# Optimization experiments

Hardware: AMD Instinct MI355X
Metric: run time of the kernel (lower is better)

The kernel has to match this reference:

```python
import jax, jax.numpy as jnp
import numpy as np

NUM_HEADS = 8


def setup_inputs() -> dict:
    key = jax.random.key(0)
    ks = jax.random.split(key, 5)
    b, c, h, w = 8, 256, 32, 32
    x = jax.random.normal(ks[0], (b, c, h, w), dtype=jnp.float32)
    w_qkv = jax.random.normal(ks[1], (3 * c, c), dtype=jnp.float32) * (c ** -0.5)
    b_qkv = jax.random.normal(ks[2], (3 * c,), dtype=jnp.float32) * 0.02
    w_proj = jax.random.normal(ks[3], (c, c), dtype=jnp.float32) * (c ** -0.5)
    b_proj = jax.random.normal(ks[4], (c,), dtype=jnp.float32) * 0.02
    return {"x": x, "w_qkv": w_qkv, "b_qkv": b_qkv, "w_proj": w_proj, "b_proj": b_proj}


def reference(x, w_qkv, b_qkv, w_proj, b_proj):
    b, c, h, w = x.shape
    nh = NUM_HEADS
    dh = c // nh
    L = h * w
    scale = dh ** -0.5
    # 1x1 conv == per-pixel GEMM
    qkv = jnp.einsum('bchw,oc->bohw', x, w_qkv) + b_qkv[None, :, None, None]
    qkv = qkv.reshape(b, 3, nh, dh, L)
    q, k, v = qkv[:, 0], qkv[:, 1], qkv[:, 2]  # each (b, nh, dh, L)
    attn = jnp.einsum('bhdi,bhdj->bhij', q, k) * scale  # (b, nh, L, L)
    attn = jax.nn.softmax(attn, axis=-1)
    out = jnp.einsum('bhdj,bhij->bhdi', v, attn)  # (b, nh, dh, L)
    out = out.reshape(b, c, h, w)
    proj = jnp.einsum('bchw,oc->bohw', out, w_proj) + b_proj[None, :, None, None]
    return x + proj
```

## Files before the change

### kernel.cpp

```cpp
#include <hip/hip_runtime.h>
#include <math.h>

#define B_   8
#define CIN  256
#define L_   1024
#define NH_  8
#define DH_  32

typedef __attribute__((ext_vector_type(8))) short short8;
typedef __attribute__((ext_vector_type(4))) short short4v;
typedef __attribute__((ext_vector_type(4))) float f32x4;
typedef __attribute__((ext_vector_type(16))) float f32x16;
typedef __attribute__((ext_vector_type(4))) unsigned int uint4v;

__device__ inline short f2bf_hu(float f) {
    union { float f; unsigned u; } v; v.f = f;
    return (short)((v.u + 0x8000u) >> 16);
}
__device__ inline float bf2f(short s) {
    union { unsigned u; float f; } v; v.u = ((unsigned)(unsigned short)s) << 16;
    return v.f;
}
__device__ inline unsigned pkbf2(float a, float b) {
    union { float f; unsigned u; } x, y; x.f = a; y.f = b;
    return __builtin_amdgcn_perm(y.u + 0x8000u, x.u + 0x8000u, 0x07060302u);
}

__global__ __launch_bounds__(256) void qkv_gemm(
    const float* __restrict__ x, const float* __restrict__ wq,
    const float* __restrict__ bias, short* __restrict__ qkv3)
{
    __shared__ __align__(16) short Xs[2][64][40];
    __shared__ __align__(16) short Wt[2][128][32];
    const int t = threadIdx.x, lane = t & 63, wv = t >> 6;
    const int n = lane & 15, quad = lane >> 4;
    const int b = blockIdx.z, o0 = blockIdx.y * 128, l0 = blockIdx.x * 64;

    float bias_r[8];
    #pragma unroll
    for (int nf = 0; nf < 8; nf++) bias_r[nf] = bias[o0 + nf * 16 + n];

    f32x4 acc[8];
    #pragma unroll
    for (int nf = 0; nf < 8; nf++) acc[nf] = (f32x4){0.f, 0.f, 0.f, 0.f};

    const int cS = t >> 3, lsS = (t & 7) * 8;

    const int ow = t >> 1, hw = t & 1;
    const float* wp = wq + (size_t)(o0 + ow) * 256 + hw * 16;
    const int wssw = (ow >> 1) & 3;
    float4 wr0, wr1, wr2, wr3;
    auto loadW = [&]() {
        wr0 = ((const float4*)wp)[0]; wr1 = ((const float4*)wp)[1];
        wr2 = ((const float4*)wp)[2]; wr3 = ((const float4*)wp)[3];
        wp += 32;
    };
    auto wwrite = [&](int buf) {
        uint4v pa = { pkbf2(wr0.x, wr0.y), pkbf2(wr0.z, wr0.w),
                      pkbf2(wr1.x, wr1.y), pkbf2(wr1.z, wr1.w) };
        uint4v pb = { pkbf2(wr2.x, wr2.y), pkbf2(wr2.z, wr2.w),
                      pkbf2(wr3.x, wr3.y), pkbf2(wr3.z, wr3.w) };
        *(uint4v*)&Wt[buf][ow][((hw * 2)     ^ wssw) * 8] = pa;
        *(uint4v*)&Wt[buf][ow][((hw * 2 + 1) ^ wssw) * 8] = pb;
    };

    auto xwrite = [&](int buf, const float4& a, const float4& c) {
        const float vals[8] = {a.x, a.y, a.z, a.w, c.x, c.y, c.z, c.w};
        #pragma unroll
        for (int k = 0; k < 8; k++) {
            const int ll = lsS + k;
            const int col = (((cS >> 3) ^ (ll & 3)) << 3) | (cS & 7);
            Xs[buf][ll][col] = f2bf_hu(vals[k]);
        }
    };

    const float* xp = &x[(((size_t)b * CIN + cS) << 10) + l0 + lsS];
    float4 xa = *(const float4*)xp, xb = *(const float4*)(xp + 4);
    loadW();
    xwrite(0, xa, xb);
    wwrite(0);
    xp += (size_t)32 << 10;
    xa = *(const float4*)xp; xb = *(const float4*)(xp + 4);
    loadW();

    const int wsw = (quad ^ ((n >> 1) & 3)) * 8;
    const int arow = wv * 16 + n;
    const int xsw = (quad ^ (arow & 3)) * 8;

    #pragma unroll
    for (int it = 0; it < 8; it++) {
        const int cur = it & 1;
        __syncthreads();
        const short8 af = *(const short8*)&Xs[cur][arow][xsw];
        #pragma unroll
        for (int nf = 0; nf < 8; nf++) {
            const short8 bf = *(const short8*)&Wt[cur][nf * 16 + n][wsw];
            acc[nf] = __builtin_amdgcn_mfma_f32_16x16x32_bf16(af, bf, acc[nf], 0, 0, 0);
        }
        if (it < 7) {
            xwrite(cur ^ 1, xa, xb);
            wwrite(cur ^ 1);
            if (it < 6) {
                xp += (size_t)32 << 10;
                xa = *(const float4*)xp; xb = *(const float4*)(xp + 4);
                loadW();
            }
        }
    }

    #pragma unroll
    for (int reg = 0; reg < 4; reg++) {
        const size_t l = l0 + wv * 16 + quad * 4 + reg;
        #pragma unroll
        for (int nf = 0; nf < 8; nf++) {
            const int o = o0 + nf * 16;
            const int tpl = o >> 8, hh = (o >> 5) & 7, dh0 = o & 31;
            short* dst = qkv3 + (((size_t)(tpl * 64 + b * 8 + hh)) << 15)
                              + l * 32 + dh0 + n;
            *dst = f2bf_hu(acc[nf][reg] + bias_r[nf]);
        }
    }
}

__global__ __launch_bounds__(256) void proj_gemm(
    const short* __restrict__ partO, const float* __restrict__ partD,
    const float* __restrict__ wq, const float* __restrict__ bias,
    const float* __restrict__ resid, float* __restrict__ out)
{
    __shared__ __align__(16) short Xs[2][64][40];
    __shared__ __align__(16) short Wt[2][64][32];
    const int t = threadIdx.x, lane = t & 63, wv = t >> 6;
    const int n = lane & 15, quad = lane >> 4;
    const int b = blockIdx.z, o0 = blockIdx.y * 64, l0 = blockIdx.x * 64;

    float bias_r[4];
    #pragma unroll
    for (int reg = 0; reg < 4; reg++) bias_r[reg] = bias[o0 + wv * 16 + quad * 4 + reg];

    f32x4 acc[4];
    #pragma unroll
    for (int nf = 0; nf < 4; nf++) acc[nf] = (f32x4){0.f, 0.f, 0.f, 0.f};

    const int l = t >> 2, cs = (t & 3) * 8;
    const size_t li = ((size_t)b << 10) + l0 + l;
    const short* p0 = &partO[(0 * (size_t)B_ * L_ + li) * CIN + cs];
    const short* p1 = &partO[(1 * (size_t)B_ * L_ + li) * CIN + cs];
    const float* pd0 = &partD[(0 * (size_t)B_ * L_ + li) * NH_];
    const float* pd1 = &partD[(1 * (size_t)B_ * L_ + li) * NH_];

    const int ow = t >> 2, cw = t & 3;
    const float* wp = wq + (size_t)(o0 + ow) * 256 + cw * 8;
    const int wpos = (cw ^ ((ow >> 1) & 3)) * 8;
    float4 wa, wb;
    auto loadW = [&]() {
        wa = ((const float4*)wp)[0]; wb = ((const float4*)wp)[1];
        wp += 32;
    };
    auto wwrite = [&](int buf) {
        uint4v pw = { pkbf2(wa.x, wa.y), pkbf2(wa.z, wa.w),
                      pkbf2(wb.x, wb.y), pkbf2(wb.z, wb.w) };
        *(uint4v*)&Wt[buf][ow][wpos] = pw;
    };

    short8 s0, s1;
    float d0, d1;
    auto combine_write = [&](int buf) {
        const float inv = 1.f / (d0 + d1);
        float v[8];
        #pragma unroll
        for (int e = 0; e < 8; e++) v[e] = (bf2f(s0[e]) + bf2f(s1[e])) * inv;
        uint4v pw = { pkbf2(v[0], v[1]), pkbf2(v[2], v[3]),
                      pkbf2(v[4], v[5]), pkbf2(v[6], v[7]) };
        *(uint4v*)&Xs[buf][l][cs] = pw;
    };

    s0 = *(const short8*)p0; s1 = *(const short8*)p1;
    d0 = pd0[0]; d1 = pd1[0];
    loadW();
    combine_write(0);
    wwrite(0);
    p0 += 32; p1 += 32;
    s0 = *(const short8*)p0; s1 = *(const short8*)p1;
    d0 = pd0[1]; d1 = pd1[1];
    loadW();

    const int wsw = (quad ^ ((n >> 1) & 3)) * 8;
    #pragma unroll
    for (int it = 0; it < 8; it++) {
        const int cur = it & 1;
        __syncthreads();
        const short8 af = *(const short8*)&Wt[cur][wv * 16 + n][wsw];
        #pragma unroll
        for (int nf = 0; nf < 4; nf++) {
            const short8 bf = *(const short8*)&Xs[cur][nf * 16 + n][quad * 8];
            acc[nf] = __builtin_amdgcn_mfma_f32_16x16x32_bf16(af, bf, acc[nf], 0, 0, 0);
        }
        if (it < 7) {
            combine_write(cur ^ 1);
            wwrite(cur ^ 1);
            if (it < 6) {
                p0 += 32; p1 += 32;
                s0 = *(const short8*)p0; s1 = *(const short8*)p1;
                d0 = pd0[it + 2]; d1 = pd1[it + 2];
                loadW();
            }
        }
    }

    #pragma unroll
    for (int reg = 0; reg < 4; reg++) {
        const int o = o0 + wv * 16 + quad * 4 + reg;
        #pragma unroll
        for (int nf = 0; nf < 4; nf++) {
            const size_t off = (((size_t)b * CIN + o) << 10) + l0 + nf * 16 + n;
            out[off] = acc[nf][reg] + bias_r[reg] + resid[off];
        }
    }
}

__global__ __launch_bounds__(256) void attn_mfma(
    const short* __restrict__ qkv3, short* __restrict__ partO,
    float* __restrict__ partD)
{
    __shared__ short Vt[2][32][80];

    const int t = threadIdx.x, lane = t & 63, wv = t >> 6;
    const int il = lane & 31, h2 = lane >> 5;
    const int id = blockIdx.x;
    const int bh = id & 63;
    const int b = bh >> 3, h = bh & 7;
    const int i0 = ((id >> 6) & 7) * 128;
    const int s  = id >> 9;

    const short* qbase = qkv3 + ((size_t)(b * 8 + h) << 15);
    const short* kbase = qbase + ((size_t)64 << 15);
    const short* vbase = qbase + ((size_t)128 << 15);

    const short* qp = qbase + (size_t)(i0 + wv * 32 + il) * 32 + h2 * 8;
    const short8 qa0 = *(const short8*)qp;
    const short8 qa1 = *(const short8*)(qp + 16);

    short8 ones;
    #pragma unroll
    for (int u = 0; u < 8; u++) ones[u] = (short)0x3F80;

    f32x16 o_acc = {0.f,0.f,0.f,0.f,0.f,0.f,0.f,0.f,
                    0.f,0.f,0.f,0.f,0.f,0.f,0.f,0.f};
    f32x16 s_acc = {0.f,0.f,0.f,0.f,0.f,0.f,0.f,0.f,
                    0.f,0.f,0.f,0.f,0.f,0.f,0.f,0.f};

    const float K1 = 0.25503510f;
    const float K2 = 11.54156036f;
    const int TSTRIDE = 64 * 32;
    const size_t soff = (size_t)s * 8 * TSTRIDE;

    const short* kp = kbase + soff + (size_t)il * 32 + h2 * 8;

    const int jS = t >> 3, dsS = (t & 7) * 4;
    const short* vp0 = vbase + soff + (size_t)jS * 32 + dsS;
    const short* vp1 = vp0 + 32 * 32;

    const int vmsk = ((dsS >> 2) & 7) << 3;
    const int vwo0 = dsS * 80 + (jS ^ vmsk);
    const int vwo1 = dsS * 80 + ((jS + 32) ^ vmsk);
    short* const vtb0 = &Vt[0][0][0];
    short* const vtb1 = &Vt[1][0][0];

    const int rmsk = ((il >> 2) & 7) << 3;
    int vro2[2][4];
    #pragma unroll
    for (int js = 0; js < 2; js++)
        #pragma unroll
        for (int g = 0; g < 4; g++)
            vro2[js][g] = il * 80 + ((js * 32 + g * 8 + 4 * h2) ^ rmsk);

    short8 kfA[4], kfB[4];

    auto stageV = [&](short* vtb) {
        const short4v a = *(const short4v*)vp0; vp0 += TSTRIDE;
        const short4v c = *(const short4v*)vp1; vp1 += TSTRIDE;
        #pragma unroll
        for (int u = 0; u < 4; u++) {
            vtb[vwo0 + u * 80] = a[u];
            vtb[vwo1 + u * 80] = c[u];
        }
    };
    auto loadK = [&](short8* kf) {
        kf[0] = *(const short8*)kp;
        kf[1] = *(const short8*)(kp + 16);
        kf[2] = *(const short8*)(kp + 1024);
        kf[3] = *(const short8*)(kp + 1024 + 16);
        kp += TSTRIDE;
    };
    auto tile = [&](const short8* kf, const short* vtb) {
        #pragma unroll
        for (int js = 0; js < 2; js++) {
            const f32x16 Z = {0.f,0.f,0.f,0.f,0.f,0.f,0.f,0.f,
                              0.f,0.f,0.f,0.f,0.f,0.f,0.f,0.f};
            f32x16 sv = __builtin_amdgcn_mfma_f32_32x32x16_bf16(kf[js*2],   qa0, Z,  0, 0, 0);
            sv        = __builtin_amdgcn_mfma_f32_32x32x16_bf16(kf[js*2+1], qa1, sv, 0, 0, 0);
            unsigned c[8];
            #pragma unroll
            for (int pi = 0; pi < 8; pi++) {
                const float pl = __builtin_amdgcn_exp2f(fmaf(sv[2*pi],   K1, -K2));
                const float ph = __builtin_amdgcn_exp2f(fmaf(sv[2*pi+1], K1, -K2));
                c[pi] = pkbf2(pl, ph);
            }
            union { unsigned u[4]; short8 s8; } pa0, pa1;
            pa0.u[0] = c[0]; pa0.u[1] = c[1]; pa0.u[2] = c[2]; pa0.u[3] = c[3];
            pa1.u[0] = c[4]; pa1.u[1] = c[5]; pa1.u[2] = c[6]; pa1.u[3] = c[7];
            union { short4v h4[2]; short8 s8; } vf0, vf1;
            vf0.h4[0] = *(const short4v*)(vtb + vro2[js][0]);
            vf0.h4[1] = *(const short4v*)(vtb + vro2[js][1]);
            o_acc = __builtin_amdgcn_mfma_f32_32x32x16_bf16(pa0.s8, vf0.s8, o_acc, 0, 0, 0);
            s_acc = __builtin_amdgcn_mfma_f32_32x32x16_bf16(pa0.s8, ones,   s_acc, 0, 0, 0);
            vf1.h4[0] = *(const short4v*)(vtb + vro2[js][2]);
            vf1.h4[1] = *(const short4v*)(vtb + vro2[js][3]);
            o_acc = __builtin_amdgcn_mfma_f32_32x32x16_bf16(pa1.s8, vf1.s8, o_acc, 0, 0, 0);
            s_acc = __builtin_amdgcn_mfma_f32_32x32x16_bf16(pa1.s8, ones,   s_acc, 0, 0, 0);
        }
    };

    stageV(vtb0);
    loadK(kfA);

    for (int itp = 0; itp < 4; itp++) {
        __syncthreads();
        stageV(vtb1);
        loadK(kfB);
        tile(kfA, vtb0);
        __syncthreads();
        if (itp < 3) { stageV(vtb0); loadK(kfA); }
        tile(kfB, vtb1);
    }

    #pragma unroll
    for (int r = 0; r < 16; r++) {
        const int irow = (r & 3) + 8 * (r >> 2) + 4 * h2;
        const int ig = i0 + wv * 32 + irow;
        partO[(((size_t)s * B_ + b) * L_ + ig) * CIN + h * DH_ + il]
            = f2bf_hu(o_acc[r]);
    }
    if (il == 0) {
        #pragma unroll
        for (int r = 0; r < 16; r++) {
            const int irow = (r & 3) + 8 * (r >> 2) + 4 * h2;
            const int ig = i0 + wv * 32 + irow;
            partD[(((size_t)s * B_ + b) * L_ + ig) * NH_ + h] = s_acc[r];
        }
    }
}

extern "C" void kernel_launch(void* const* d_in, const int* in_sizes, int n_in,
                              void* d_out, int out_size, void* d_ws, size_t ws_size,
                              hipStream_t stream) {
    const float* x      = (const float*)d_in[0];
    const float* w_qkv  = (const float*)d_in[1];
    const float* b_qkv  = (const float*)d_in[2];
    const float* w_proj = (const float*)d_in[3];
    const float* b_proj = (const float*)d_in[4];
    float* out = (float*)d_out;

    short* qkv3  = (short*)d_ws;
    short* partO = qkv3 + (size_t)B_ * L_ * 768;
    float* partD = (float*)(partO + (size_t)2 * B_ * L_ * CIN);

    qkv_gemm<<<dim3(16, 6, B_), 256, 0, stream>>>(x, w_qkv, b_qkv, qkv3);
    attn_mfma<<<dim3(1024), 256, 0, stream>>>(qkv3, partO, partD);
    proj_gemm<<<dim3(16, 4, B_), 256, 0, stream>>>(partO, partD, w_proj,
                                                   b_proj, x, out);
}
```

Baseline: 106.3 us.

## Store V transposed from QKV GEMM and read it directly in attention

The QKV GEMM epilogue now writes the V third in a transposed (dh-major, L contiguous) layout using 4-wide vector stores. The attention kernel then loads V fragments straight from global memory, which removes the LDS staging buffer, the transposing scatter and both __syncthreads per iteration. The cost is more global and L2 traffic for V reads, with 8-byte loads per lane instead of shared-memory reuse across waves.

```diff
diff --git a/kernel.cpp b/kernel.cpp
--- a/kernel.cpp
+++ b/kernel.cpp
@@ -108,16 +108,30 @@
         }
     }
 
-    #pragma unroll
-    for (int reg = 0; reg < 4; reg++) {
-        const size_t l = l0 + wv * 16 + quad * 4 + reg;
+    if (o0 < 512) {
+        #pragma unroll
+        for (int reg = 0; reg < 4; reg++) {
+            const size_t l = l0 + wv * 16 + quad * 4 + reg;
+            #pragma unroll
+            for (int nf = 0; nf < 8; nf++) {
+                const int o = o0 + nf * 16;
+                const int tpl = o >> 8, hh = (o >> 5) & 7, dh0 = o & 31;
+                short* dst = qkv3 + (((size_t)(tpl * 64 + b * 8 + hh)) << 15)
+                                  + l * 32 + dh0 + n;
+                *dst = f2bf_hu(acc[nf][reg] + bias_r[nf]);
+            }
+        }
+    } else {
         #pragma unroll
         for (int nf = 0; nf < 8; nf++) {
             const int o = o0 + nf * 16;
-            const int tpl = o >> 8, hh = (o >> 5) & 7, dh0 = o & 31;
-            short* dst = qkv3 + (((size_t)(tpl * 64 + b * 8 + hh)) << 15)
-                              + l * 32 + dh0 + n;
-            *dst = f2bf_hu(acc[nf][reg] + bias_r[nf]);
+            const int hh = (o >> 5) & 7, dh = (o & 31) + n;
+            short4v s4;
+            #pragma unroll
+            for (int reg = 0; reg < 4; reg++)
+                s4[reg] = f2bf_hu(acc[nf][reg] + bias_r[nf]);
+            *(short4v*)(qkv3 + ((size_t)(128 + b * 8 + hh) << 15)
+                        + (size_t)dh * 1024 + l0 + wv * 16 + quad * 4) = s4;
         }
     }
 }
@@ -222,8 +236,6 @@
     const short* __restrict__ qkv3, short* __restrict__ partO,
     float* __restrict__ partD)
 {
-    __shared__ short Vt[2][32][80];
-
     const int t = threadIdx.x, lane = t & 63, wv = t >> 6;
     const int il = lane & 31, h2 = lane >> 5;
     const int id = blockIdx.x;
@@ -234,7 +246,7 @@
 
     const short* qbase = qkv3 + ((size_t)(b * 8 + h) << 15);
     const short* kbase = qbase + ((size_t)64 << 15);
-    const short* vbase = qbase + ((size_t)128 << 15);
+    const short* vbase = qkv3 + ((size_t)(128 + b * 8 + h) << 15);
 
     const short* qp = qbase + (size_t)(i0 + wv * 32 + il) * 32 + h2 * 8;
     const short8 qa0 = *(const short8*)qp;
@@ -256,35 +268,10 @@
 
     const short* kp = kbase + soff + (size_t)il * 32 + h2 * 8;
 
-    const int jS = t >> 3, dsS = (t & 7) * 4;
-    const short* vp0 = vbase + soff + (size_t)jS * 32 + dsS;
-    const short* vp1 = vp0 + 32 * 32;
-
-    const int vmsk = ((dsS >> 2) & 7) << 3;
-    const int vwo0 = dsS * 80 + (jS ^ vmsk);
-    const int vwo1 = dsS * 80 + ((jS + 32) ^ vmsk);
-    short* const vtb0 = &Vt[0][0][0];
-    short* const vtb1 = &Vt[1][0][0];
-
-    const int rmsk = ((il >> 2) & 7) << 3;
-    int vro2[2][4];
-    #pragma unroll
-    for (int js = 0; js < 2; js++)
-        #pragma unroll
-        for (int g = 0; g < 4; g++)
-            vro2[js][g] = il * 80 + ((js * 32 + g * 8 + 4 * h2) ^ rmsk);
+    const short* vrow = vbase + (size_t)il * 1024 + s * 512 + 4 * h2;
 
     short8 kfA[4], kfB[4];
 
-    auto stageV = [&](short* vtb) {
-        const short4v a = *(const short4v*)vp0; vp0 += TSTRIDE;
-        const short4v c = *(const short4v*)vp1; vp1 += TSTRIDE;
-        #pragma unroll
-        for (int u = 0; u < 4; u++) {
-            vtb[vwo0 + u * 80] = a[u];
-            vtb[vwo1 + u * 80] = c[u];
-        }
-    };
     auto loadK = [&](short8* kf) {
         kf[0] = *(const short8*)kp;
         kf[1] = *(const short8*)(kp + 16);
@@ -292,9 +279,17 @@
         kf[3] = *(const short8*)(kp + 1024 + 16);
         kp += TSTRIDE;
     };
-    auto tile = [&](const short8* kf, const short* vtb) {
+    auto tile = [&](const short8* kf, int jt) {
+        const int jb = jt * 64;
         #pragma unroll
         for (int js = 0; js < 2; js++) {
+            const short* vr = vrow + jb + js * 32;
+            union { short4v h4[2]; short8 s8; } vf0, vf1;
+            vf0.h4[0] = *(const short4v*)(vr);
+            vf0.h4[1] = *(const short4v*)(vr + 8);
+            vf1.h4[0] = *(const short4v*)(vr + 16);
+            vf1.h4[1] = *(const short4v*)(vr + 24);
+
             const f32x16 Z = {0.f,0.f,0.f,0.f,0.f,0.f,0.f,0.f,
                               0.f,0.f,0.f,0.f,0.f,0.f,0.f,0.f};
             f32x16 sv = __builtin_amdgcn_mfma_f32_32x32x16_bf16(kf[js*2],   qa0, Z,  0, 0, 0);
@@ -309,29 +304,23 @@
             union { unsigned u[4]; short8 s8; } pa0, pa1;
             pa0.u[0] = c[0]; pa0.u[1] = c[1]; pa0.u[2] = c[2]; pa0.u[3] = c[3];
             pa1.u[0] = c[4]; pa1.u[1] = c[5]; pa1.u[2] = c[6]; pa1.u[3] = c[7];
-            union { short4v h4[2]; short8 s8; } vf0, vf1;
-            vf0.h4[0] = *(const short4v*)(vtb + vro2[js][0]);
-            vf0.h4[1] = *(const short4v*)(vtb + vro2[js][1]);
             o_acc = __builtin_amdgcn_mfma_f32_32x32x16_bf16(pa0.s8, vf0.s8, o_acc, 0, 0, 0);
             s_acc = __builtin_amdgcn_mfma_f32_32x32x16_bf16(pa0.s8, ones,   s_acc, 0, 0, 0);
-            vf1.h4[0] = *(const short4v*)(vtb + vro2[js][2]);
-            vf1.h4[1] = *(const short4v*)(vtb + vro2[js][3]);
             o_acc = __builtin_amdgcn_mfma_f32_32x32x16_bf16(pa1.s8, vf1.s8, o_acc, 0, 0, 0);
             s_acc = __builtin_amdgcn_mfma_f32_32x32x16_bf16(pa1.s8, ones,   s_acc, 0, 0, 0);
         }
     };
 
-    stageV(vtb0);
     loadK(kfA);
-
-    for (int itp = 0; itp < 4; itp++) {
-        __syncthreads();
-        stageV(vtb1);
-        loadK(kfB);
-        tile(kfA, vtb0);
-        __syncthreads();
-        if (itp < 3) { stageV(vtb0); loadK(kfA); }
-        tile(kfB, vtb1);
+    #pragma unroll
+    for (int jt = 0; jt < 8; jt++) {
+        if ((jt & 1) == 0) {
+            if (jt < 7) loadK(kfB);
+            tile(kfA, jt);
+        } else {
+            if (jt < 7) loadK(kfA);
+            tile(kfB, jt);
+        }
     }
 
     #pragma unroll
```

Result: slower. 125.5 us (+18.1%).
